# Performance work log

Hardware: AMD Instinct MI355X
Metric: run time of the kernel (lower is better)

## Reference

```python
import jax, jax.numpy as jnp
import numpy as np

N = 100000       # nodes
E_RAND = 3200000  # random edges; + N self loops appended
F_IN = 128
D = 64
SUBHEADS = 2
ALPHA = 0.2  # leaky_relu negative slope


def setup_inputs() -> dict:
    key = jax.random.key(0)
    ks = jax.random.split(key, 8)
    x = jax.random.normal(ks[0], (N, F_IN), jnp.float32)
    src = jax.random.randint(ks[1], (E_RAND,), 0, N)
    dst = jax.random.randint(ks[2], (E_RAND,), 0, N)
    loops = jnp.arange(N)  # add_remaining_self_loops
    edge_index = jnp.stack([jnp.concatenate([src, loops]),
                            jnp.concatenate([dst, loops])])  # [2, E_RAND+N]
    # xavier_normal_(gain=1.414): std = gain*sqrt(2/(fan_in+fan_out))
    xav = lambda k, shp, fan: jax.random.normal(k, shp, jnp.float32) * np.float32(1.414 * np.sqrt(2.0 / fan))
    W = xav(ks[3], (SUBHEADS, F_IN, D), F_IN + D)     # per-subhead weight
    b = jnp.zeros((SUBHEADS, D), jnp.float32)          # per-subhead bias
    fc = xav(ks[4], (SUBHEADS, D, 1), D + 1)           # NodeAdaptiveEncoder.fc
    bf = jnp.zeros((SUBHEADS,), jnp.float32)           # NodeAdaptiveEncoder.bf
    a_src = xav(ks[5], (SUBHEADS, D), D + 1)           # attention vector (dst side)
    a_dst = xav(ks[6], (SUBHEADS, D), D + 1)           # attention vector (src side)
    return dict(x=x, edge_index=edge_index, W=W, b=b, fc=fc, bf=bf, a_src=a_src, a_dst=a_dst)


def reference(x, edge_index, W, b, fc, bf, a_src, a_dst):
    row, col = edge_index[0], edge_index[1]  # out[row] += val * h[col]
    n = x.shape[0]
    outs = []
    for i in range(SUBHEADS):
        h = x @ W[i]  # [N, D]; dropout is identity in eval mode
        # --- GAT-style edge attention over the sparse graph ---
        s_r = h @ a_src[i]  # [N]
        s_c = h @ a_dst[i]  # [N]
        e = jax.nn.leaky_relu(s_r[row] + s_c[col], ALPHA)  # [E]
        m = jax.ops.segment_max(e, row, num_segments=n)
        ee = jnp.exp(e - m[row])
        denom = jax.ops.segment_sum(ee, row, num_segments=n)
        att = ee / denom[row]  # adj_mat_val = ones * softmax(e)
        # --- row normalization ---
        rs = jax.ops.segment_sum(att, row, num_segments=n)
        val = att / jnp.where(rs == 0, 1.0, rs)[row]
        # --- (i+1) hops of spmm ---
        vh = h
        for _ in range(i + 1):
            vh = jax.ops.segment_sum(val[:, None] * vh[col], row, num_segments=n)
        vh = jnp.where(jnp.isnan(vh), 0.0, vh)  # val_h[val_h != val_h] = 0
        vh = vh + b[i]
        # --- NodeAdaptiveEncoder: relu(x) + sigmoid(x@fc+bf) * min(x, 0) ---
        g = jax.nn.sigmoid(vh @ fc[i] + bf[i])  # [N, 1]
        vh = jnp.maximum(vh, 0.0) + g * jnp.minimum(vh, 0.0)
        vh = jax.nn.leaky_relu(vh, ALPHA)  # activation
        outs.append(vh)
    return jnp.concatenate(outs, axis=1)  # [N, SUBHEADS*D]
```

## Files before the change

kernel.cpp:

```cpp
#include <hip/hip_runtime.h>

#define ALPHA 0.2f

typedef short bf16x8 __attribute__((ext_vector_type(8)));
typedef float f32x4  __attribute__((ext_vector_type(4)));

__device__ __forceinline__ unsigned short f2bf(float f) {
    unsigned u = __float_as_uint(f);
    u += 0x7FFFu + ((u >> 16) & 1u);
    return (unsigned short)(u >> 16);
}
__device__ __forceinline__ float bflo(unsigned u) {
    return __uint_as_float(u << 16);
}
__device__ __forceinline__ float bfhi(unsigned u) {
    return __uint_as_float(u & 0xFFFF0000u);
}


__global__ __launch_bounds__(256) void f17_p1(
    const int* __restrict__ row, const int* __restrict__ col, int E, int N,
    int B, int CH, int* __restrict__ hist,
    const float* __restrict__ W, unsigned short* __restrict__ WT)
{
    __shared__ int h[4096];
    const int b = blockIdx.x, t = threadIdx.x;
    for (int k = t; k < B; k += 256) h[k] = 0;
    int gidx = b * 256 + t;
    if (gidx < 16384) {
        int i = gidx >> 13, c = (gidx >> 7) & 63, kk = gidx & 127;
        WT[gidx] = f2bf(W[i * 8192 + kk * 64 + c]);
    }
    __syncthreads();
    long base = (long)b * CH;
    long end  = base + CH; if (end > E) end = E;
    for (long e = base + t; e < end; e += 256) {
        int r = row[e], c = col[e];
        if ((unsigned)r < (unsigned)N && (unsigned)c < (unsigned)N)
            atomicAdd(&h[r >> 5], 1);
    }
    __syncthreads();
    for (int k = t; k < B; k += 256) hist[(size_t)k * 256 + b] = h[k];
}

__global__ __launch_bounds__(256) void f17_sc1(
    const int* __restrict__ h, int* __restrict__ bsums, int M)
{
    __shared__ int sdat[256];
    int t = threadIdx.x, blk = blockIdx.x;
    long base = (long)blk * 4096 + t * 16;
    int s = 0;
    #pragma unroll
    for (int j = 0; j < 16; ++j) {
        long idx = base + j;
        if (idx < M) s += h[idx];
    }
    sdat[t] = s; __syncthreads();
    for (int o = 1; o < 256; o <<= 1) {
        int add = (t >= o) ? sdat[t - o] : 0;
        __syncthreads();
        sdat[t] += add;
        __syncthreads();
    }
    if (t == 255) bsums[blk] = sdat[255];
}
__global__ __launch_bounds__(256) void f8_scan2(
    const int* __restrict__ bsums, int* __restrict__ boffs, int nb)
{
    __shared__ int sdat[256];
    int t = threadIdx.x;
    int v = (t < nb) ? bsums[t] : 0;
    sdat[t] = v; __syncthreads();
    for (int o = 1; o < 256; o <<= 1) {
        int add = (t >= o) ? sdat[t - o] : 0;
        __syncthreads();
// ... 6 lines not shown
    int* __restrict__ h, const int* __restrict__ boffs,
    int* __restrict__ bstart, int M)
{
    __shared__ int sdat[256];
    int t = threadIdx.x, blk = blockIdx.x;
    long base = (long)blk * 4096 + t * 16;
    int v[16]; int s = 0;
    #pragma unroll
    for (int j = 0; j < 16; ++j) {
        long idx = base + j;
        v[j] = (idx < M) ? h[idx] : 0;
        s += v[j];
    }
    sdat[t] = s; __syncthreads();
    for (int o = 1; o < 256; o <<= 1) {
        int add = (t >= o) ? sdat[t - o] : 0;
        __syncthreads();
        sdat[t] += add;
        __syncthreads();
    }
    int excl = boffs[blk] + sdat[t] - s;
    #pragma unroll
    for (int j = 0; j < 16; ++j) {
        long idx = base + j;
        if (idx < M) {
            h[idx] = excl;
            if ((idx & 255) == 0) bstart[idx >> 8] = excl;
            if (idx == M - 1)     bstart[M >> 8]   = excl + v[j];
            excl += v[j];
        }
    }
}

__global__ __launch_bounds__(256) void f17_p2(
    const int* __restrict__ row, const int* __restrict__ col, int E, int N,
    int B, int CH, const int* __restrict__ hist,
    const float* __restrict__ s_r, const float* __restrict__ s_c,
    uint2* __restrict__ pkA)
{
    __shared__ int cur[4096];
    const int b = blockIdx.x, t = threadIdx.x;
    for (int k = t; k < B; k += 256) cur[k] = hist[(size_t)k * 256 + b];
    __syncthreads();
    long base = (long)b * CH;
    long end  = base + CH; if (end > E) end = E;
    for (long e = base + t; e < end; e += 256) {
        int r = row[e], c = col[e];
        if ((unsigned)r >= (unsigned)N || (unsigned)c >= (unsigned)N) continue;
        float e0 = s_r[r] + s_c[c];
        float e1 = s_r[(size_t)N + r] + s_c[(size_t)N + c];
        e0 = (e0 > 0.f) ? e0 : ALPHA * e0;
        e1 = (e1 > 0.f) ? e1 : ALPHA * e1;
        unsigned py = ((unsigned)f2bf(expf(e1)) << 16) | (unsigned)f2bf(expf(e0));
        int pos = atomicAdd(&cur[r >> 5], 1);
        uint2 m; m.x = (unsigned)c | ((unsigned)(r & 31) << 25); m.y = py;
        pkA[pos] = m;
    }
}

__global__ __launch_bounds__(256) void f17_p3(
    const uint2* __restrict__ pkA, const int* __restrict__ bstart,
    int N, int B, uint2* __restrict__ pkB, int* __restrict__ rp)
{
    __shared__ int h32[32], ex33[33], cur32[32];
    const int k = blockIdx.x, t = threadIdx.x;
    const int p0 = bstart[k], p1 = bstart[k + 1];
    if (t < 32) h32[t] = 0;
    __syncthreads();
    for (int p = p0 + t; p < p1; p += 256)
        atomicAdd(&h32[pkA[p].x >> 25], 1);
    __syncthreads();
    if (t == 0) {
        int s = 0;
        #pragma unroll
        for (int j = 0; j < 32; ++j) { ex33[j] = s; s += h32[j]; }
        ex33[32] = s;
    }
    __syncthreads();
    if (t < 32) {
        int r = k * 32 + t;
        if (r < N) rp[r] = p0 + ex33[t];
        cur32[t] = p0 + ex33[t];
    }
    if (k == B - 1 && t == 0) rp[N] = p1;
    __syncthreads();
    for (int p = p0 + t; p < p1; p += 256) {
        uint2 m = pkA[p];
        int pos = atomicAdd(&cur32[m.x >> 25], 1);
        uint2 o; o.x = m.x & 0x01FFFFFFu; o.y = m.y;
        pkB[pos] = o;
    }
}

__global__ __launch_bounds__(256) void f14_h(
    const float* __restrict__ x,
    const unsigned short* __restrict__ WT,
    const float* __restrict__ a_src, const float* __restrict__ a_dst,
    unsigned short* __restrict__ Hb,
    float* __restrict__ s_r, float* __restrict__ s_c, int N)
{
    __shared__ __align__(16) unsigned short hs[4][16][72];
    const int t  = threadIdx.x;
    const int wv = t >> 6, l = t & 63;
    const int i  = blockIdx.x & 1;
    const int n0 = (blockIdx.x >> 1) * 64 + wv * 16;
    const int lm = l & 15, lg = l >> 4;

    int arow = n0 + lm; if (arow >= N) arow = N - 1;
    const float* xr = x + (size_t)arow * 128 + lg * 8;
    bf16x8 af[4];
    #pragma unroll
    for (int ks = 0; ks < 4; ++ks) {
        float4 u0 = *(const float4*)(xr + ks * 32);
        float4 u1 = *(const float4*)(xr + ks * 32 + 4);
        bf16x8 a;
        a[0] = (short)f2bf(u0.x); a[1] = (short)f2bf(u0.y);
        a[2] = (short)f2bf(u0.z); a[3] = (short)f2bf(u0.w);
        a[4] = (short)f2bf(u1.x); a[5] = (short)f2bf(u1.y);
        a[6] = (short)f2bf(u1.z); a[7] = (short)f2bf(u1.w);
        af[ks] = a;
    }

    const unsigned short* wr = WT + ((size_t)i * 64 + lm) * 128 + lg * 8;
    f32x4 zero = {0.f, 0.f, 0.f, 0.f};
    f32x4 acc[4];
    #pragma unroll
    for (int ct = 0; ct < 4; ++ct) {
        acc[ct] = zero;
        #pragma unroll
        for (int ks = 0; ks < 4; ++ks) {
            bf16x8 bf = *(const bf16x8*)(wr + ct * 16 * 128 + ks * 32);
            acc[ct] = __builtin_amdgcn_mfma_f32_16x16x32_bf16(af[ks], bf, acc[ct], 0, 0, 0);
        }
    }

    float asv[4], adv[4];
    #pragma unroll
    for (int ct = 0; ct < 4; ++ct) {
        asv[ct] = a_src[i * 64 + ct * 16 + lm];
        adv[ct] = a_dst[i * 64 + ct * 16 + lm];
    }
    #pragma unroll
    for (int reg = 0; reg < 4; ++reg) {
        float vr = 0.f, vc = 0.f;
        #pragma unroll
        for (int ct = 0; ct < 4; ++ct) {
            vr = fmaf(acc[ct][reg], asv[ct], vr);
            vc = fmaf(acc[ct][reg], adv[ct], vc);
        }
        #pragma unroll
        for (int off = 8; off; off >>= 1) {
            vr += __shfl_xor(vr, off);
            vc += __shfl_xor(vc, off);
        }
        int n = n0 + lg * 4 + reg;
        if (lm == 0 && n < N) {
            s_r[(size_t)i * N + n] = vr;
            s_c[(size_t)i * N + n] = vc;
        }
    }

    #pragma unroll
    for (int ct = 0; ct < 4; ++ct)
        #pragma unroll
        for (int reg = 0; reg < 4; ++reg)
            hs[wv][lg * 4 + reg][ct * 16 + lm] = f2bf(acc[ct][reg]);
    #pragma unroll
    for (int j = 0; j < 2; ++j) {
        int r = (l >> 3) + j * 8;
        int n = n0 + r;
        if (n < N) {
            int g = (l & 7) * 8;
            *(uint4*)(Hb + (size_t)n * 128 + i * 64 + g) =
                *(const uint4*)&hs[wv][r][g];
        }
    }
}

__global__ __launch_bounds__(256) void f10_h(
    const float* __restrict__ x, const float* __restrict__ W,
    const float* __restrict__ a_src, const float* __restrict__ a_dst,
    const int* __restrict__ row, const int* __restrict__ col, int E,
    int* __restrict__ cnt,
    float* __restrict__ Hf, unsigned short* __restrict__ Hb,
    float* __restrict__ s_r, float* __restrict__ s_c, int N)
{
    __shared__ __align__(16) float ws[128][64];
    __shared__ __align__(16) float xs[128][36];
    const int t  = threadIdx.x;
    const int i  = blockIdx.x & 1;
    const int n0 = (blockIdx.x >> 1) * 32;

    if (cnt) {
        const long total = (long)gridDim.x * 256;
        for (long e = (long)blockIdx.x * 256 + t; e < E; e += total) {
            int r = row[e], c = col[e];
            if ((unsigned)r < (unsigned)N && (unsigned)c < (unsigned)N)
                atomicAdd(cnt + r, 1);
        }
    }
    {
        const float* wp = W + (size_t)i * 8192;
        #pragma unroll
        for (int j = 0; j < 8; ++j) {
            int idx = t + j * 256;
            int k   = idx >> 4;
            int c4  = (idx & 15) * 4;
            *(float4*)&ws[k][c4] = *(const float4*)(wp + k * 64 + c4);
        }
    }
    {
        int r = t >> 3;
        int n = n0 + r;
        #pragma unroll
        for (int j = 0; j < 4; ++j) {
            int k0 = ((t & 7) + j * 8) * 4;
            float4 v = (n < N) ? *(const float4*)(x + (size_t)n * 128 + k0)
                               : make_float4(0.f, 0.f, 0.f, 0.f);
            xs[k0 + 0][r] = v.x; xs[k0 + 1][r] = v.y;
            xs[k0 + 2][r] = v.z; xs[k0 + 3][r] = v.w;
        }
    }
    __syncthreads();

    const int tc = t & 31, tn = t >> 5;
    float acc[4][2] = {};
    #pragma unroll 8
    for (int k = 0; k < 128; ++k) {
        float4 xv = *(const float4*)&xs[k][tn * 4];
        float2 wv = *(const float2*)&ws[k][tc * 2];
        acc[0][0] = fmaf(xv.x, wv.x, acc[0][0]);
        acc[0][1] = fmaf(xv.x, wv.y, acc[0][1]);
        acc[1][0] = fmaf(xv.y, wv.x, acc[1][0]);
        acc[1][1] = fmaf(xv.y, wv.y, acc[1][1]);
        acc[2][0] = fmaf(xv.z, wv.x, acc[2][0]);
        acc[2][1] = fmaf(xv.z, wv.y, acc[2][1]);
        acc[3][0] = fmaf(xv.w, wv.x, acc[3][0]);
        acc[3][1] = fmaf(xv.w, wv.y, acc[3][1]);
    }

    const float2 asv = *(const float2*)(a_src + i * 64 + tc * 2);
    const float2 adv = *(const float2*)(a_dst + i * 64 + tc * 2);
    #pragma unroll
    for (int a = 0; a < 4; ++a) {
        int n = n0 + tn * 4 + a;
        if (n >= N) break;
        float2 hv; hv.x = acc[a][0]; hv.y = acc[a][1];
        if (Hf) *(float2*)(Hf + (size_t)n * 128 + i * 64 + tc * 2) = hv;
        if (Hb) {
            ushort2 hb; hb.x = f2bf(hv.x); hb.y = f2bf(hv.y);
            *(ushort2*)(Hb + (size_t)n * 128 + (i * 32 + tc) * 2) = hb;
        }
        float pr = hv.x * asv.x + hv.y * asv.y;
        float pc = hv.x * adv.x + hv.y * adv.y;
        #pragma unroll
        for (int off = 16; off; off >>= 1) {
            pr += __shfl_xor(pr, off);
            pc += __shfl_xor(pc, off);
        }
        if (tc == 0) {
            s_r[(size_t)i * N + n] = pr;
            s_c[(size_t)i * N + n] = pc;
        }
    }
}

__global__ __launch_bounds__(256) void f16_scan1(
    const int* __restrict__ cnt, int* __restrict__ bsums, int N, int cs)
{
    __shared__ int sdat[256];
    int t = threadIdx.x, b = blockIdx.x;
    int s = 0;
    #pragma unroll
    for (int j = 0; j < 4; ++j) {
        int idx = b * 1024 + t * 4 + j;
        if (idx < N) s += cnt[(size_t)idx * cs];
    }
    sdat[t] = s; __syncthreads();
    for (int o = 1; o < 256; o <<= 1) {
        int add = (t >= o) ? sdat[t - o] : 0;
        __syncthreads();
        sdat[t] += add;
        __syncthreads();
    }
    if (t == 255) bsums[b] = sdat[255];
}
__global__ __launch_bounds__(256) void f16_scan3(
    int* __restrict__ cnt, const int* __restrict__ boffs,
    int* __restrict__ rp, int N, int cs)
{
    __shared__ int sdat[256];
    int t = threadIdx.x, b = blockIdx.x;
    int v[4]; int s = 0;
    #pragma unroll
    for (int j = 0; j < 4; ++j) {
        int idx = b * 1024 + t * 4 + j;
        v[j] = (idx < N) ? cnt[(size_t)idx * cs] : 0;
        s += v[j];
    }
    sdat[t] = s; __syncthreads();
    for (int o = 1; o < 256; o <<= 1) {
        int add = (t >= o) ? sdat[t - o] : 0;
        __syncthreads();
        sdat[t] += add;
        __syncthreads();
    }
    int excl = boffs[b] + sdat[t] - s;
    #pragma unroll
    for (int j = 0; j < 4; ++j) {
        int idx = b * 1024 + t * 4 + j;
        if (idx < N) {
            rp[idx] = excl;
            if (cs == 1) cnt[idx] = excl;
            if (idx == N - 1) rp[N] = excl + v[j];
            excl += v[j];
        }
    }
}

__global__ __launch_bounds__(256) void f8_scatter(
    const int* __restrict__ row, const int* __restrict__ col, int E,
    int* __restrict__ cur, int* __restrict__ colp, int N)
{
    int e = blockIdx.x * 256 + threadIdx.x;
    if (e >= E) return;
    int r = row[e], c = col[e];
    if ((unsigned)r >= (unsigned)N || (unsigned)c >= (unsigned)N) return;
    int pos = atomicAdd(cur + r, 1);
    colp[pos] = c;
}

__global__ __launch_bounds__(256) void f12_spmm2(
    const int* __restrict__ rp, const uint2* __restrict__ pk,
    const unsigned* __restrict__ Hb,
    const float* __restrict__ b, const float* __restrict__ fc,
    const float* __restrict__ bfv,
    unsigned short* __restrict__ A1b, float* __restrict__ out, int N)
{
    long gid = (long)blockIdx.x * 256 + threadIdx.x;
    int r = (int)(gid >> 6), d = (int)(gid & 63);
    if (r >= N) return;
    int p0 = rp[r], p1 = rp[r + 1];
    const int sub = d >> 5;
    float a0 = 0.f, a1 = 0.f, den = 0.f;
    int p = p0;
    for (; p + 8 <= p1; p += 8) {
        uint2 m0 = pk[p],     m1 = pk[p + 1], m2 = pk[p + 2], m3 = pk[p + 3];
        uint2 m4 = pk[p + 4], m5 = pk[p + 5], m6 = pk[p + 6], m7 = pk[p + 7];
        unsigned u0 = Hb[(size_t)m0.x * 64 + d];
        unsigned u1 = Hb[(size_t)m1.x * 64 + d];
        unsigned u2 = Hb[(size_t)m2.x * 64 + d];
        unsigned u3 = Hb[(size_t)m3.x * 64 + d];
        unsigned u4 = Hb[(size_t)m4.x * 64 + d];
        unsigned u5 = Hb[(size_t)m5.x * 64 + d];
        unsigned u6 = Hb[(size_t)m6.x * 64 + d];
        unsigned u7 = Hb[(size_t)m7.x * 64 + d];
        float v0 = sub ? bfhi(m0.y) : bflo(m0.y);
        float v1 = sub ? bfhi(m1.y) : bflo(m1.y);
        float v2 = sub ? bfhi(m2.y) : bflo(m2.y);
        float v3 = sub ? bfhi(m3.y) : bflo(m3.y);
        float v4 = sub ? bfhi(m4.y) : bflo(m4.y);
        float v5 = sub ? bfhi(m5.y) : bflo(m5.y);
        float v6 = sub ? bfhi(m6.y) : bflo(m6.y);
        float v7 = sub ? bfhi(m7.y) : bflo(m7.y);
        a0 = fmaf(v0, bflo(u0), a0); a1 = fmaf(v0, bfhi(u0), a1); den += v0;
        a0 = fmaf(v1, bflo(u1), a0); a1 = fmaf(v1, bfhi(u1), a1); den += v1;
        a0 = fmaf(v2, bflo(u2), a0); a1 = fmaf(v2, bfhi(u2), a1); den += v2;
        a0 = fmaf(v3, bflo(u3), a0); a1 = fmaf(v3, bfhi(u3), a1); den += v3;
        a0 = fmaf(v4, bflo(u4), a0); a1 = fmaf(v4, bfhi(u4), a1); den += v4;
        a0 = fmaf(v5, bflo(u5), a0); a1 = fmaf(v5, bfhi(u5), a1); den += v5;
        a0 = fmaf(v6, bflo(u6), a0); a1 = fmaf(v6, bfhi(u6), a1); den += v6;
        a0 = fmaf(v7, bflo(u7), a0); a1 = fmaf(v7, bfhi(u7), a1); den += v7;
    }
    for (; p < p1; ++p) {
        uint2 m = pk[p];
        unsigned u = Hb[(size_t)m.x * 64 + d];
        float v = sub ? bfhi(m.y) : bflo(m.y);
        a0 = fmaf(v, bflo(u), a0); a1 = fmaf(v, bfhi(u), a1); den += v;
    }
    float inv = (p1 > p0) ? 1.f / den : 0.f;
    float r0 = a0 * inv, r1 = a1 * inv;
    if (sub) {
        ushort2 res; res.x = f2bf(r0); res.y = f2bf(r1);
        *(ushort2*)(A1b + (size_t)r * 64 + (d - 32) * 2) = res;
    } else {
        int dcol = 2 * d;
        float vh0 = (r0 != r0) ? 0.f : r0;
        float vh1 = (r1 != r1) ? 0.f : r1;
        float2 bb = *(const float2*)(b + dcol);
        float2 ff = *(const float2*)(fc + dcol);
        vh0 += bb.x; vh1 += bb.y;
        float pp = vh0 * ff.x + vh1 * ff.y;
        #pragma unroll
        for (int off = 16; off; off >>= 1) pp += __shfl_xor(pp, off);
        float g = 1.f / (1.f + expf(-(pp + bfv[0])));
        float q0 = fmaxf(vh0, 0.f) + g * fminf(vh0, 0.f);
        float q1 = fmaxf(vh1, 0.f) + g * fminf(vh1, 0.f);
        q0 = (q0 > 0.f) ? q0 : ALPHA * q0;
        q1 = (q1 > 0.f) ? q1 : ALPHA * q1;
        float2 res; res.x = q0; res.y = q1;
        *(float2*)(out + (size_t)r * 128 + dcol) = res;
    }
}

__global__ __launch_bounds__(256) void f16_fin2(
    const int* __restrict__ rp, const uint2* __restrict__ pk,
    const unsigned* __restrict__ A1u,
    const float* __restrict__ b, const float* __restrict__ fc,
    const float* __restrict__ bfv,
    float* __restrict__ out, int N)
{
    long gid = (long)blockIdx.x * 256 + threadIdx.x;
    int r = (int)(gid >> 6), l = (int)(gid & 63);
    if (r >= N) return;
    const int half = l >> 5, lh = l & 31;
    int p0 = rp[r], p1 = rp[r + 1];
    float a0 = 0.f, a1 = 0.f, den = 0.f;
    int p = p0;
    for (; p + 8 <= p1; p += 8) {
        uint2 m0 = pk[p + half],     m1 = pk[p + 2 + half];
        uint2 m2 = pk[p + 4 + half], m3 = pk[p + 6 + half];
        unsigned u0 = A1u[(size_t)m0.x * 32 + lh];
        unsigned u1 = A1u[(size_t)m1.x * 32 + lh];
        unsigned u2 = A1u[(size_t)m2.x * 32 + lh];
        unsigned u3 = A1u[(size_t)m3.x * 32 + lh];
        float v0 = bfhi(m0.y), v1 = bfhi(m1.y);
        float v2 = bfhi(m2.y), v3 = bfhi(m3.y);
        a0 = fmaf(v0, bflo(u0), a0); a1 = fmaf(v0, bfhi(u0), a1); den += v0;
        a0 = fmaf(v1, bflo(u1), a0); a1 = fmaf(v1, bfhi(u1), a1); den += v1;
        a0 = fmaf(v2, bflo(u2), a0); a1 = fmaf(v2, bfhi(u2), a1); den += v2;
        a0 = fmaf(v3, bflo(u3), a0); a1 = fmaf(v3, bfhi(u3), a1); den += v3;
    }
    for (; p + 2 <= p1; p += 2) {
        uint2 m = pk[p + half];
        unsigned u = A1u[(size_t)m.x * 32 + lh];
        float v = bfhi(m.y);
        a0 = fmaf(v, bflo(u), a0); a1 = fmaf(v, bfhi(u), a1); den += v;
    }
    if (p < p1 && half == 0) {
        uint2 m = pk[p];
        unsigned u = A1u[(size_t)m.x * 32 + lh];
        float v = bfhi(m.y);
        a0 = fmaf(v, bflo(u), a0); a1 = fmaf(v, bfhi(u), a1); den += v;
    }
    a0 += __shfl_xor(a0, 32);
    a1 += __shfl_xor(a1, 32);
    den += __shfl_xor(den, 32);

    float inv = (p1 > p0) ? 1.f / den : 0.f;
    float vh0 = a0 * inv, vh1 = a1 * inv;
    if (vh0 != vh0) vh0 = 0.f;
    if (vh1 != vh1) vh1 = 0.f;
    const int dcol = 64 + 2 * lh;
    vh0 += b[dcol]; vh1 += b[dcol + 1];
    float pp = vh0 * fc[dcol] + vh1 * fc[dcol + 1];
    #pragma unroll
    for (int off = 16; off; off >>= 1) pp += __shfl_xor(pp, off);
    float g = 1.f / (1.f + expf(-(pp + bfv[1])));
    float q0 = fmaxf(vh0, 0.f) + g * fminf(vh0, 0.f);
    float q1 = fmaxf(vh1, 0.f) + g * fminf(vh1, 0.f);
    q0 = (q0 > 0.f) ? q0 : ALPHA * q0;
    q1 = (q1 > 0.f) ? q1 : ALPHA * q1;
    if (half == 0) {
        float2 res; res.x = q0; res.y = q1;
        *(float2*)(out + (size_t)r * 128 + dcol) = res;
    }
}

__global__ __launch_bounds__(256) void f11_spmm2_cp(
    const int* __restrict__ rp, const int* __restrict__ colp,
    const float* __restrict__ s_r, const float* __restrict__ s_c,
    const float* __restrict__ H,
    float* __restrict__ A0, float* __restrict__ A1, int N)
{
    long gid = (long)blockIdx.x * 256 + threadIdx.x;
    int r = (int)(gid >> 6), d = (int)(gid & 63);
    if (r >= N) return;
    int p0 = rp[r], p1 = rp[r + 1];
    const int sub = d >> 5;
    const float* scp = s_c + (size_t)sub * N;
    float sr = s_r[(size_t)sub * N + r];
    const float2* H2 = (const float2*)H;
    float a0 = 0.f, a1 = 0.f, den = 0.f;
    int p = p0;
    for (; p + 4 <= p1; p += 4) {
        int c0 = colp[p], c1 = colp[p + 1], c2 = colp[p + 2], c3 = colp[p + 3];
        float sc0 = scp[c0], sc1 = scp[c1], sc2 = scp[c2], sc3 = scp[c3];
        float2 h0 = H2[(size_t)c0 * 64 + d];
        float2 h1 = H2[(size_t)c1 * 64 + d];
        float2 h2 = H2[(size_t)c2 * 64 + d];
        float2 h3 = H2[(size_t)c3 * 64 + d];
        float e0 = sr + sc0; e0 = (e0 > 0.f) ? e0 : ALPHA * e0; float v0 = expf(e0);
        float e1 = sr + sc1; e1 = (e1 > 0.f) ? e1 : ALPHA * e1; float v1 = expf(e1);
        float e2 = sr + sc2; e2 = (e2 > 0.f) ? e2 : ALPHA * e2; float v2 = expf(e2);
        float e3 = sr + sc3; e3 = (e3 > 0.f) ? e3 : ALPHA * e3; float v3 = expf(e3);
        a0 = fmaf(v0, h0.x, a0); a1 = fmaf(v0, h0.y, a1); den += v0;
        a0 = fmaf(v1, h1.x, a0); a1 = fmaf(v1, h1.y, a1); den += v1;
        a0 = fmaf(v2, h2.x, a0); a1 = fmaf(v2, h2.y, a1); den += v2;
        a0 = fmaf(v3, h3.x, a0); a1 = fmaf(v3, h3.y, a1); den += v3;
// ... 132 lines not shown
}

extern "C" void kernel_launch(void* const* d_in, const int* in_sizes, int n_in,
                              void* d_out, int out_size, void* d_ws, size_t ws_size,
                              hipStream_t stream) {
    const float* x     = (const float*)d_in[0];
    const int*   ei    = (const int*)d_in[1];
    const float* W     = (const float*)d_in[2];
    const float* b     = (const float*)d_in[3];
    const float* fc    = (const float*)d_in[4];
    const float* bfv   = (const float*)d_in[5];
    const float* a_src = (const float*)d_in[6];
    const float* a_dst = (const float*)d_in[7];
    float* out = (float*)d_out;

    const int N = in_sizes[0] / 128;
    const int E = in_sizes[1] / 2;
    const int* row = ei;
    const int* col = ei + E;
    (void)n_in; (void)out_size;

    const int B  = (N + 31) >> 5;
    const int M  = B * 256;
    const int CH = (E + 255) / 256;
    const int nbh = (M + 4095) / 4096;

    unsigned short* Hb   = (unsigned short*)d_ws;
    unsigned short* A1b  = Hb + (size_t)N * 128;
    unsigned short* WT   = A1b + (size_t)N * 64;
    uint2*          pkA  = (uint2*)(WT + 16384);
    uint2*          pkB  = pkA + E;
    int*            hist = (int*)(pkB + E);
    int*            bst  = hist + (size_t)M;
    float*          s_rP = (float*)(bst + (B + 1));
    float*          s_cP = s_rP + 2 * (size_t)N;
    int*            rpP  = (int*)(s_cP + 2 * (size_t)N);
    int*            bsumP = rpP + (N + 1);
    int*            boffP = bsumP + 256;
    size_t          needP = (size_t)((char*)(boffP + 256) - (char*)d_ws);

    float* A0a   = (float*)d_ws;
    float* A1a   = A0a + (size_t)N * 64;
    int*   colpA = (int*)(A1a + (size_t)N * 64);
    float* s_rA  = (float*)(colpA + E);
    float* s_cA  = s_rA + 2 * (size_t)N;
    int*   rpA   = (int*)(s_cA + 2 * (size_t)N);
    int*   cntA  = rpA + (N + 1);
    int*   bsumA = cntA + N;
    int*   boffA = bsumA + 256;
    size_t needA = (size_t)((char*)(boffA + 256) - (char*)d_ws);

    const int g10 = 2 * ((N + 31) / 32);
    const int g14 = 2 * ((N + 63) / 64);
    const int eb  = (E + 255) / 256;
    const int rb  = (int)(((long)N * 64 + 255) / 256);
    const int nb  = (N + 1023) / 1024;

    if (ws_size >= needP && B <= 4096 && nbh <= 256) {
        f17_p1<<<256, 256, 0, stream>>>(row, col, E, N, B, CH, hist, W, WT);
        f14_h<<<g14, 256, 0, stream>>>(x, WT, a_src, a_dst, Hb, s_rP, s_cP, N);
        f17_sc1<<<nbh, 256, 0, stream>>>(hist, bsumP, M);
        f8_scan2<<<1, 256, 0, stream>>>(bsumP, boffP, nbh);
        f17_sc3<<<nbh, 256, 0, stream>>>(hist, boffP, bst, M);
        f17_p2<<<256, 256, 0, stream>>>(row, col, E, N, B, CH, hist,
                                        s_rP, s_cP, pkA);
        f17_p3<<<B, 256, 0, stream>>>(pkA, bst, N, B, pkB, rpP);
        f12_spmm2<<<rb, 256, 0, stream>>>(rpP, pkB, (const unsigned*)Hb,
                                          b, fc, bfv, A1b, out, N);
        f16_fin2<<<rb, 256, 0, stream>>>(rpP, pkB, (const unsigned*)A1b,
                                         b, fc, bfv, out, N);
    } else if (ws_size >= needA) {
        hipMemsetAsync(cntA, 0, (size_t)N * sizeof(int), stream);
        f10_h<<<g10, 256, 0, stream>>>(x, W, a_src, a_dst, row, col, E, cntA,
                                       out, nullptr, s_rA, s_cA, N);
        f16_scan1<<<nb, 256, 0, stream>>>(cntA, bsumA, N, 1);
        f8_scan2<<<1, 256, 0, stream>>>(bsumA, boffA, nb);
        f16_scan3<<<nb, 256, 0, stream>>>(cntA, boffA, rpA, N, 1);
        f8_scatter<<<eb, 256, 0, stream>>>(row, col, E, cntA, colpA, N);
        f11_spmm2_cp<<<rb, 256, 0, stream>>>(rpA, colpA, s_rA, s_cA, out,
                                             A0a, A1a, N);
        f8_fin<<<rb, 256, 0, stream>>>(A0a, b, fc, bfv, out, N, 0);
        f9_spmm_fin<<<rb, 256, 0, stream>>>(rpA, colpA, s_rA + N, s_cA + N,
                                            A1a, 64, 0, b, fc, bfv, out, N, 1);
    } else {
        float* A     = (float*)d_ws;
        float* s_r   = A + (size_t)N * 64;
        float* s_c   = s_r + 2 * (size_t)N;
        float* denom = s_c + 2 * (size_t)N;
        const size_t planeB = (size_t)N * 64 * sizeof(float);
        const int sb = (int)(((((long)E + 7) / 8) * 64 + 255) / 256);
        hipMemsetAsync(denom, 0, 2 * (size_t)N * sizeof(float), stream);
        f10_h<<<g10, 256, 0, stream>>>(x, W, a_src, a_dst, row, col, E, nullptr,
                                       out, nullptr, s_r, s_c, N);
        f8_edge<<<eb, 256, 0, stream>>>(row, col, E, s_r, s_c, denom, nullptr, N);
        const float* s_r1 = s_r + N; const float* s_c1 = s_c + N; const float* den1 = denom + N;
        hipMemsetAsync(A, 0, planeB, stream);
        f7_spmm<<<sb, 256, 0, stream>>>(row, col, E, s_r, s_c, denom, out, 0, A, N);
        f8_fin<<<rb, 256, 0, stream>>>(A, b, fc, bfv, out, N, 0);
        hipMemsetAsync(A, 0, planeB, stream);
        f7_spmm<<<sb, 256, 0, stream>>>(row, col, E, s_r1, s_c1, den1, out, 64, A, N);
        f7_copy<<<rb, 256, 0, stream>>>(A, out, 64, N);
        hipMemsetAsync(A, 0, planeB, stream);
        f7_spmm<<<sb, 256, 0, stream>>>(row, col, E, s_r1, s_c1, den1, out, 64, A, N);
// ... 4 lines not shown
```

Before: 512.9 us.

## Fuse edge histogram into projection kernel and precompute softmax denominators in bucket pass

Merges the edge-row histogram pass and the MFMA projection into one launch: the first 256 blocks build the histogram and the rest compute H, so the two independent stages can overlap, and the weight transpose moves to its own small kernel. The per-subhead attention scores are interleaved as float2 per node, so the edge pass fetches both heads with one load per endpoint. The softmax denominators are now summed once in the row-bucket sort kernel with shared-memory float atomics and stored per row. The two SpMM kernels read that value instead of re-accumulating and shuffle-reducing it. The cost is extra shared atomics in the bucket pass, and the denominator is summed in a different order.

```diff
diff --git a/kernel.cpp b/kernel.cpp
--- a/kernel.cpp
+++ b/kernel.cpp
@@ -17,30 +17,121 @@
     return __uint_as_float(u & 0xFFFF0000u);
 }
 
-
-__global__ __launch_bounds__(256) void f17_p1(
-    const int* __restrict__ row, const int* __restrict__ col, int E, int N,
-    int B, int CH, int* __restrict__ hist,
+__global__ __launch_bounds__(256) void f15_wt(
     const float* __restrict__ W, unsigned short* __restrict__ WT)
 {
-    __shared__ int h[4096];
-    const int b = blockIdx.x, t = threadIdx.x;
-    for (int k = t; k < B; k += 256) h[k] = 0;
-    int gidx = b * 256 + t;
-    if (gidx < 16384) {
-        int i = gidx >> 13, c = (gidx >> 7) & 63, kk = gidx & 127;
-        WT[gidx] = f2bf(W[i * 8192 + kk * 64 + c]);
-    }
-    __syncthreads();
-    long base = (long)b * CH;
-    long end  = base + CH; if (end > E) end = E;
-    for (long e = base + t; e < end; e += 256) {
-        int r = row[e], c = col[e];
-        if ((unsigned)r < (unsigned)N && (unsigned)c < (unsigned)N)
-            atomicAdd(&h[r >> 5], 1);
-    }
-    __syncthreads();
-    for (int k = t; k < B; k += 256) hist[(size_t)k * 256 + b] = h[k];
+    int t = blockIdx.x * 256 + threadIdx.x;
+    if (t < 2 * 64 * 128) {
+        int i = t >> 13, c = (t >> 7) & 63, k = t & 127;
+        WT[t] = f2bf(W[i * 8192 + k * 64 + c]);
+    }
+}
+
+__global__ __launch_bounds__(256) void f18_h(
+    const float* __restrict__ x,
+    const unsigned short* __restrict__ WT,
+    const float* __restrict__ a_src, const float* __restrict__ a_dst,
+    const int* __restrict__ row, const int* __restrict__ col, int E,
+    int N, int B, int CH, int* __restrict__ hist,
+    unsigned short* __restrict__ Hb,
+    float* __restrict__ s2_r, float* __restrict__ s2_c)
+{
+    __shared__ __align__(16) unsigned char sm[16384];
+    const int t = threadIdx.x;
+
+    if (blockIdx.x < 256) {
+        int* h = (int*)sm;
+        const int b = blockIdx.x;
+        for (int k = t; k < B; k += 256) h[k] = 0;
+        __syncthreads();
+        long base = (long)b * CH;
+        long end  = base + CH; if (end > E) end = E;
+        for (long e = base + t; e < end; e += 256) {
+            int r = row[e], c = col[e];
+            if ((unsigned)r < (unsigned)N && (unsigned)c < (unsigned)N)
+                atomicAdd(&h[r >> 5], 1);
+        }
+        __syncthreads();
+        for (int k = t; k < B; k += 256) hist[(size_t)k * 256 + b] = h[k];
+        return;
+    }
+
+    unsigned short (*hs)[16][72] = (unsigned short (*)[16][72])sm;
+    const int bid = blockIdx.x - 256;
+    const int wv = t >> 6, l = t & 63;
+    const int i  = bid & 1;
+    const int n0 = (bid >> 1) * 64 + wv * 16;
+    const int lm = l & 15, lg = l >> 4;
+
+    int arow = n0 + lm; if (arow >= N) arow = N - 1;
+    const float* xr = x + (size_t)arow * 128 + lg * 8;
+    bf16x8 af[4];
+    #pragma unroll
+    for (int ks = 0; ks < 4; ++ks) {
+        float4 u0 = *(const float4*)(xr + ks * 32);
+        float4 u1 = *(const float4*)(xr + ks * 32 + 4);
+        bf16x8 a;
+        a[0] = (short)f2bf(u0.x); a[1] = (short)f2bf(u0.y);
+        a[2] = (short)f2bf(u0.z); a[3] = (short)f2bf(u0.w);
+        a[4] = (short)f2bf(u1.x); a[5] = (short)f2bf(u1.y);
+        a[6] = (short)f2bf(u1.z); a[7] = (short)f2bf(u1.w);
+        af[ks] = a;
+    }
+
+    const unsigned short* wr = WT + ((size_t)i * 64 + lm) * 128 + lg * 8;
+    f32x4 zero = {0.f, 0.f, 0.f, 0.f};
+    f32x4 acc[4];
+    #pragma unroll
+    for (int ct = 0; ct < 4; ++ct) {
+        acc[ct] = zero;
+        #pragma unroll
+        for (int ks = 0; ks < 4; ++ks) {
+            bf16x8 bf = *(const bf16x8*)(wr + ct * 16 * 128 + ks * 32);
+            acc[ct] = __builtin_amdgcn_mfma_f32_16x16x32_bf16(af[ks], bf, acc[ct], 0, 0, 0);
+        }
+    }
+
+    float asv[4], adv[4];
+    #pragma unroll
+    for (int ct = 0; ct < 4; ++ct) {
+        asv[ct] = a_src[i * 64 + ct * 16 + lm];
+        adv[ct] = a_dst[i * 64 + ct * 16 + lm];
+    }
+    #pragma unroll
+    for (int reg = 0; reg < 4; ++reg) {
+        float vr = 0.f, vc = 0.f;
+        #pragma unroll
+        for (int ct = 0; ct < 4; ++ct) {
+            vr = fmaf(acc[ct][reg], asv[ct], vr);
+            vc = fmaf(acc[ct][reg], adv[ct], vc);
+        }
+        #pragma unroll
+        for (int off = 8; off; off >>= 1) {
+            vr += __shfl_xor(vr, off);
+            vc += __shfl_xor(vc, off);
+        }
+        int n = n0 + lg * 4 + reg;
+        if (lm == 0 && n < N) {
+            s2_r[(size_t)n * 2 + i] = vr;
+            s2_c[(size_t)n * 2 + i] = vc;
+        }
+    }
+
+    #pragma unroll
+    for (int ct = 0; ct < 4; ++ct)
+        #pragma unroll
+        for (int reg = 0; reg < 4; ++reg)
+            hs[wv][lg * 4 + reg][ct * 16 + lm] = f2bf(acc[ct][reg]);
+    #pragma unroll
+    for (int j = 0; j < 2; ++j) {
+        int r = (l >> 3) + j * 8;
+        int n = n0 + r;
+        if (n < N) {
+            int g = (l & 7) * 8;
+            *(uint4*)(Hb + (size_t)n * 128 + i * 64 + g) =
+                *(const uint4*)&hs[wv][r][g];
+        }
+    }
 }
 
 __global__ __launch_bounds__(256) void f17_sc1(
@@ -113,10 +204,10 @@
     }
 }
 
-__global__ __launch_bounds__(256) void f17_p2(
+__global__ __launch_bounds__(256) void f18_p2(
     const int* __restrict__ row, const int* __restrict__ col, int E, int N,
     int B, int CH, const int* __restrict__ hist,
-    const float* __restrict__ s_r, const float* __restrict__ s_c,
+    const float* __restrict__ s2_r, const float* __restrict__ s2_c,
     uint2* __restrict__ pkA)
 {
     __shared__ int cur[4096];
@@ -128,8 +219,10 @@
     for (long e = base + t; e < end; e += 256) {
         int r = row[e], c = col[e];
         if ((unsigned)r >= (unsigned)N || (unsigned)c >= (unsigned)N) continue;
-        float e0 = s_r[r] + s_c[c];
-        float e1 = s_r[(size_t)N + r] + s_c[(size_t)N + c];
+        float2 sr = *(const float2*)(s2_r + (size_t)r * 2);
+        float2 sc = *(const float2*)(s2_c + (size_t)c * 2);
+        float e0 = sr.x + sc.x;
+        float e1 = sr.y + sc.y;
         e0 = (e0 > 0.f) ? e0 : ALPHA * e0;
         e1 = (e1 > 0.f) ? e1 : ALPHA * e1;
         unsigned py = ((unsigned)f2bf(expf(e1)) << 16) | (unsigned)f2bf(expf(e0));
@@ -139,17 +232,24 @@
     }
 }
 
-__global__ __launch_bounds__(256) void f17_p3(
+__global__ __launch_bounds__(256) void f18_p3(
     const uint2* __restrict__ pkA, const int* __restrict__ bstart,
-    int N, int B, uint2* __restrict__ pkB, int* __restrict__ rp)
+    int N, int B, uint2* __restrict__ pkB, int* __restrict__ rp,
+    float* __restrict__ den2)
 {
     __shared__ int h32[32], ex33[33], cur32[32];
+    __shared__ float d0[32], d1[32];
     const int k = blockIdx.x, t = threadIdx.x;
     const int p0 = bstart[k], p1 = bstart[k + 1];
-    if (t < 32) h32[t] = 0;
+    if (t < 32) { h32[t] = 0; d0[t] = 0.f; d1[t] = 0.f; }
     __syncthreads();
-    for (int p = p0 + t; p < p1; p += 256)
-        atomicAdd(&h32[pkA[p].x >> 25], 1);
+    for (int p = p0 + t; p < p1; p += 256) {
+        uint2 m = pkA[p];
+        int rl = m.x >> 25;
+        atomicAdd(&h32[rl], 1);
+        atomicAdd(&d0[rl], bflo(m.y));
+        atomicAdd(&d1[rl], bfhi(m.y));
+    }
     __syncthreads();
     if (t == 0) {
         int s = 0;
@@ -160,7 +260,11 @@
     __syncthreads();
     if (t < 32) {
         int r = k * 32 + t;
-        if (r < N) rp[r] = p0 + ex33[t];
+        if (r < N) {
+            rp[r] = p0 + ex33[t];
+            float2 dd; dd.x = d0[t]; dd.y = d1[t];
+            *(float2*)(den2 + (size_t)r * 2) = dd;
+        }
         cur32[t] = p0 + ex33[t];
     }
     if (k == B - 1 && t == 0) rp[N] = p1;
@@ -173,247 +277,10 @@
     }
 }
 
-__global__ __launch_bounds__(256) void f14_h(
-    const float* __restrict__ x,
-    const unsigned short* __restrict__ WT,
-    const float* __restrict__ a_src, const float* __restrict__ a_dst,
-    unsigned short* __restrict__ Hb,
-    float* __restrict__ s_r, float* __restrict__ s_c, int N)
-{
-    __shared__ __align__(16) unsigned short hs[4][16][72];
-    const int t  = threadIdx.x;
-    const int wv = t >> 6, l = t & 63;
-    const int i  = blockIdx.x & 1;
-    const int n0 = (blockIdx.x >> 1) * 64 + wv * 16;
-    const int lm = l & 15, lg = l >> 4;
-
-    int arow = n0 + lm; if (arow >= N) arow = N - 1;
-    const float* xr = x + (size_t)arow * 128 + lg * 8;
-    bf16x8 af[4];
-    #pragma unroll
-    for (int ks = 0; ks < 4; ++ks) {
-        float4 u0 = *(const float4*)(xr + ks * 32);
-        float4 u1 = *(const float4*)(xr + ks * 32 + 4);
-        bf16x8 a;
-        a[0] = (short)f2bf(u0.x); a[1] = (short)f2bf(u0.y);
-        a[2] = (short)f2bf(u0.z); a[3] = (short)f2bf(u0.w);
-        a[4] = (short)f2bf(u1.x); a[5] = (short)f2bf(u1.y);
-        a[6] = (short)f2bf(u1.z); a[7] = (short)f2bf(u1.w);
-        af[ks] = a;
-    }
-
-    const unsigned short* wr = WT + ((size_t)i * 64 + lm) * 128 + lg * 8;
-    f32x4 zero = {0.f, 0.f, 0.f, 0.f};
-    f32x4 acc[4];
-    #pragma unroll
-    for (int ct = 0; ct < 4; ++ct) {
-        acc[ct] = zero;
-        #pragma unroll
-        for (int ks = 0; ks < 4; ++ks) {
-            bf16x8 bf = *(const bf16x8*)(wr + ct * 16 * 128 + ks * 32);
-            acc[ct] = __builtin_amdgcn_mfma_f32_16x16x32_bf16(af[ks], bf, acc[ct], 0, 0, 0);
-        }
-    }
-
-    float asv[4], adv[4];
-    #pragma unroll
-    for (int ct = 0; ct < 4; ++ct) {
-        asv[ct] = a_src[i * 64 + ct * 16 + lm];
-        adv[ct] = a_dst[i * 64 + ct * 16 + lm];
-    }
-    #pragma unroll
-    for (int reg = 0; reg < 4; ++reg) {
-        float vr = 0.f, vc = 0.f;
-        #pragma unroll
-        for (int ct = 0; ct < 4; ++ct) {
-            vr = fmaf(acc[ct][reg], asv[ct], vr);
-            vc = fmaf(acc[ct][reg], adv[ct], vc);
-        }
-        #pragma unroll
-        for (int off = 8; off; off >>= 1) {
-            vr += __shfl_xor(vr, off);
-            vc += __shfl_xor(vc, off);
-        }
-        int n = n0 + lg * 4 + reg;
-        if (lm == 0 && n < N) {
-            s_r[(size_t)i * N + n] = vr;
-            s_c[(size_t)i * N + n] = vc;
-        }
-    }
-
-    #pragma unroll
-    for (int ct = 0; ct < 4; ++ct)
-        #pragma unroll
-        for (int reg = 0; reg < 4; ++reg)
-            hs[wv][lg * 4 + reg][ct * 16 + lm] = f2bf(acc[ct][reg]);
-    #pragma unroll
-    for (int j = 0; j < 2; ++j) {
-        int r = (l >> 3) + j * 8;
-        int n = n0 + r;
-        if (n < N) {
-            int g = (l & 7) * 8;
-            *(uint4*)(Hb + (size_t)n * 128 + i * 64 + g) =
-                *(const uint4*)&hs[wv][r][g];
-        }
-    }
-}
-
-__global__ __launch_bounds__(256) void f10_h(
-    const float* __restrict__ x, const float* __restrict__ W,
-    const float* __restrict__ a_src, const float* __restrict__ a_dst,
-    const int* __restrict__ row, const int* __restrict__ col, int E,
-    int* __restrict__ cnt,
-    float* __restrict__ Hf, unsigned short* __restrict__ Hb,
-    float* __restrict__ s_r, float* __restrict__ s_c, int N)
-{
-    __shared__ __align__(16) float ws[128][64];
-    __shared__ __align__(16) float xs[128][36];
-    const int t  = threadIdx.x;
-    const int i  = blockIdx.x & 1;
-    const int n0 = (blockIdx.x >> 1) * 32;
-
-    if (cnt) {
-        const long total = (long)gridDim.x * 256;
-        for (long e = (long)blockIdx.x * 256 + t; e < E; e += total) {
-            int r = row[e], c = col[e];
-            if ((unsigned)r < (unsigned)N && (unsigned)c < (unsigned)N)
-                atomicAdd(cnt + r, 1);
-        }
-    }
-    {
-        const float* wp = W + (size_t)i * 8192;
-        #pragma unroll
-        for (int j = 0; j < 8; ++j) {
-            int idx = t + j * 256;
-            int k   = idx >> 4;
-            int c4  = (idx & 15) * 4;
-            *(float4*)&ws[k][c4] = *(const float4*)(wp + k * 64 + c4);
-        }
-    }
-    {
-        int r = t >> 3;
-        int n = n0 + r;
-        #pragma unroll
-        for (int j = 0; j < 4; ++j) {
-            int k0 = ((t & 7) + j * 8) * 4;
-            float4 v = (n < N) ? *(const float4*)(x + (size_t)n * 128 + k0)
-                               : make_float4(0.f, 0.f, 0.f, 0.f);
-            xs[k0 + 0][r] = v.x; xs[k0 + 1][r] = v.y;
-            xs[k0 + 2][r] = v.z; xs[k0 + 3][r] = v.w;
-        }
-    }
-    __syncthreads();
-
-    const int tc = t & 31, tn = t >> 5;
-    float acc[4][2] = {};
-    #pragma unroll 8
-    for (int k = 0; k < 128; ++k) {
-        float4 xv = *(const float4*)&xs[k][tn * 4];
-        float2 wv = *(const float2*)&ws[k][tc * 2];
-        acc[0][0] = fmaf(xv.x, wv.x, acc[0][0]);
-        acc[0][1] = fmaf(xv.x, wv.y, acc[0][1]);
-        acc[1][0] = fmaf(xv.y, wv.x, acc[1][0]);
-        acc[1][1] = fmaf(xv.y, wv.y, acc[1][1]);
-        acc[2][0] = fmaf(xv.z, wv.x, acc[2][0]);
-        acc[2][1] = fmaf(xv.z, wv.y, acc[2][1]);
-        acc[3][0] = fmaf(xv.w, wv.x, acc[3][0]);
-        acc[3][1] = fmaf(xv.w, wv.y, acc[3][1]);
-    }
-
-    const float2 asv = *(const float2*)(a_src + i * 64 + tc * 2);
-    const float2 adv = *(const float2*)(a_dst + i * 64 + tc * 2);
-    #pragma unroll
-    for (int a = 0; a < 4; ++a) {
-        int n = n0 + tn * 4 + a;
-        if (n >= N) break;
-        float2 hv; hv.x = acc[a][0]; hv.y = acc[a][1];
-        if (Hf) *(float2*)(Hf + (size_t)n * 128 + i * 64 + tc * 2) = hv;
-        if (Hb) {
-            ushort2 hb; hb.x = f2bf(hv.x); hb.y = f2bf(hv.y);
-            *(ushort2*)(Hb + (size_t)n * 128 + (i * 32 + tc) * 2) = hb;
-        }
-        float pr = hv.x * asv.x + hv.y * asv.y;
-        float pc = hv.x * adv.x + hv.y * adv.y;
-        #pragma unroll
-        for (int off = 16; off; off >>= 1) {
-            pr += __shfl_xor(pr, off);
-            pc += __shfl_xor(pc, off);
-        }
-        if (tc == 0) {
-            s_r[(size_t)i * N + n] = pr;
-            s_c[(size_t)i * N + n] = pc;
-        }
-    }
-}
-
-__global__ __launch_bounds__(256) void f16_scan1(
-    const int* __restrict__ cnt, int* __restrict__ bsums, int N, int cs)
-{
-    __shared__ int sdat[256];
-    int t = threadIdx.x, b = blockIdx.x;
-    int s = 0;
-    #pragma unroll
-    for (int j = 0; j < 4; ++j) {
-        int idx = b * 1024 + t * 4 + j;
-        if (idx < N) s += cnt[(size_t)idx * cs];
-    }
-    sdat[t] = s; __syncthreads();
-    for (int o = 1; o < 256; o <<= 1) {
-        int add = (t >= o) ? sdat[t - o] : 0;
-        __syncthreads();
-        sdat[t] += add;
-        __syncthreads();
-    }
-    if (t == 255) bsums[b] = sdat[255];
-}
-__global__ __launch_bounds__(256) void f16_scan3(
-    int* __restrict__ cnt, const int* __restrict__ boffs,
-    int* __restrict__ rp, int N, int cs)
-{
-    __shared__ int sdat[256];
-    int t = threadIdx.x, b = blockIdx.x;
-    int v[4]; int s = 0;
-    #pragma unroll
-    for (int j = 0; j < 4; ++j) {
-        int idx = b * 1024 + t * 4 + j;
-        v[j] = (idx < N) ? cnt[(size_t)idx * cs] : 0;
-        s += v[j];
-    }
-    sdat[t] = s; __syncthreads();
-    for (int o = 1; o < 256; o <<= 1) {
-        int add = (t >= o) ? sdat[t - o] : 0;
-        __syncthreads();
-        sdat[t] += add;
-        __syncthreads();
-    }
-    int excl = boffs[b] + sdat[t] - s;
-    #pragma unroll
-    for (int j = 0; j < 4; ++j) {
-        int idx = b * 1024 + t * 4 + j;
-        if (idx < N) {
-            rp[idx] = excl;
-            if (cs == 1) cnt[idx] = excl;
-            if (idx == N - 1) rp[N] = excl + v[j];
-            excl += v[j];
-        }
-    }
-}
-
-__global__ __launch_bounds__(256) void f8_scatter(
-    const int* __restrict__ row, const int* __restrict__ col, int E,
-    int* __restrict__ cur, int* __restrict__ colp, int N)
-{
-    int e = blockIdx.x * 256 + threadIdx.x;
-    if (e >= E) return;
-    int r = row[e], c = col[e];
-    if ((unsigned)r >= (unsigned)N || (unsigned)c >= (unsigned)N) return;
-    int pos = atomicAdd(cur + r, 1);
-    colp[pos] = c;
-}
-
-__global__ __launch_bounds__(256) void f12_spmm2(
+__global__ __launch_bounds__(256) void f18_spmm2(
     const int* __restrict__ rp, const uint2* __restrict__ pk,
     const unsigned* __restrict__ Hb,
+    const float* __restrict__ den2,
     const float* __restrict__ b, const float* __restrict__ fc,
     const float* __restrict__ bfv,
     unsigned short* __restrict__ A1b, float* __restrict__ out, int N)
@@ -423,7 +290,8 @@
     if (r >= N) return;
     int p0 = rp[r], p1 = rp[r + 1];
     const int sub = d >> 5;
-    float a0 = 0.f, a1 = 0.f, den = 0.f;
+    float den = den2[(size_t)r * 2 + sub];
+    float a0 = 0.f, a1 = 0.f;
     int p = p0;
     for (; p + 8 <= p1; p += 8) {
         uint2 m0 = pk[p],     m1 = pk[p + 1], m2 = pk[p + 2], m3 = pk[p + 3];
@@ -444,20 +312,20 @@
         float v5 = sub ? bfhi(m5.y) : bflo(m5.y);
         float v6 = sub ? bfhi(m6.y) : bflo(m6.y);
         float v7 = sub ? bfhi(m7.y) : bflo(m7.y);
-        a0 = fmaf(v0, bflo(u0), a0); a1 = fmaf(v0, bfhi(u0), a1); den += v0;
-        a0 = fmaf(v1, bflo(u1), a0); a1 = fmaf(v1, bfhi(u1), a1); den += v1;
-        a0 = fmaf(v2, bflo(u2), a0); a1 = fmaf(v2, bfhi(u2), a1); den += v2;
-        a0 = fmaf(v3, bflo(u3), a0); a1 = fmaf(v3, bfhi(u3), a1); den += v3;
-        a0 = fmaf(v4, bflo(u4), a0); a1 = fmaf(v4, bfhi(u4), a1); den += v4;
-        a0 = fmaf(v5, bflo(u5), a0); a1 = fmaf(v5, bfhi(u5), a1); den += v5;
-        a0 = fmaf(v6, bflo(u6), a0); a1 = fmaf(v6, bfhi(u6), a1); den += v6;
-        a0 = fmaf(v7, bflo(u7), a0); a1 = fmaf(v7, bfhi(u7), a1); den += v7;
+        a0 = fmaf(v0, bflo(u0), a0); a1 = fmaf(v0, bfhi(u0), a1);
+        a0 = fmaf(v1, bflo(u1), a0); a1 = fmaf(v1, bfhi(u1), a1);
+        a0 = fmaf(v2, bflo(u2), a0); a1 = fmaf(v2, bfhi(u2), a1);
+        a0 = fmaf(v3, bflo(u3), a0); a1 = fmaf(v3, bfhi(u3), a1);
+        a0 = fmaf(v4, bflo(u4), a0); a1 = fmaf(v4, bfhi(u4), a1);
+        a0 = fmaf(v5, bflo(u5), a0); a1 = fmaf(v5, bfhi(u5), a1);
+        a0 = fmaf(v6, bflo(u6), a0); a1 = fmaf(v6, bfhi(u6), a1);
+        a0 = fmaf(v7, bflo(u7), a0); a1 = fmaf(v7, bfhi(u7), a1);
     }
     for (; p < p1; ++p) {
         uint2 m = pk[p];
         unsigned u = Hb[(size_t)m.x * 64 + d];
         float v = sub ? bfhi(m.y) : bflo(m.y);
-        a0 = fmaf(v, bflo(u), a0); a1 = fmaf(v, bfhi(u), a1); den += v;
+        a0 = fmaf(v, bflo(u), a0); a1 = fmaf(v, bfhi(u), a1);
     }
     float inv = (p1 > p0) ? 1.f / den : 0.f;
     float r0 = a0 * inv, r1 = a1 * inv;
@@ -484,9 +352,10 @@
     }
 }
 
-__global__ __launch_bounds__(256) void f16_fin2(
+__global__ __launch_bounds__(256) void f18_fin2(
     const int* __restrict__ rp, const uint2* __restrict__ pk,
     const unsigned* __restrict__ A1u,
+    const float* __restrict__ den2,
     const float* __restrict__ b, const float* __restrict__ fc,
     const float* __restrict__ bfv,
     float* __restrict__ out, int N)
@@ -496,7 +365,8 @@
     if (r >= N) return;
     const int half = l >> 5, lh = l & 31;
     int p0 = rp[r], p1 = rp[r + 1];
-    float a0 = 0.f, a1 = 0.f, den = 0.f;
+    float den = den2[(size_t)r * 2 + 1];
+    float a0 = 0.f, a1 = 0.f;
     int p = p0;
     for (; p + 8 <= p1; p += 8) {
         uint2 m0 = pk[p + half],     m1 = pk[p + 2 + half];
@@ -507,26 +377,25 @@
         unsigned u3 = A1u[(size_t)m3.x * 32 + lh];
         float v0 = bfhi(m0.y), v1 = bfhi(m1.y);
         float v2 = bfhi(m2.y), v3 = bfhi(m3.y);
-        a0 = fmaf(v0, bflo(u0), a0); a1 = fmaf(v0, bfhi(u0), a1); den += v0;
-        a0 = fmaf(v1, bflo(u1), a0); a1 = fmaf(v1, bfhi(u1), a1); den += v1;
-        a0 = fmaf(v2, bflo(u2), a0); a1 = fmaf(v2, bfhi(u2), a1); den += v2;
-        a0 = fmaf(v3, bflo(u3), a0); a1 = fmaf(v3, bfhi(u3), a1); den += v3;
+        a0 = fmaf(v0, bflo(u0), a0); a1 = fmaf(v0, bfhi(u0), a1);
+        a0 = fmaf(v1, bflo(u1), a0); a1 = fmaf(v1, bfhi(u1), a1);
+        a0 = fmaf(v2, bflo(u2), a0); a1 = fmaf(v2, bfhi(u2), a1);
+        a0 = fmaf(v3, bflo(u3), a0); a1 = fmaf(v3, bfhi(u3), a1);
     }
     for (; p + 2 <= p1; p += 2) {
         uint2 m = pk[p + half];
         unsigned u = A1u[(size_t)m.x * 32 + lh];
         float v = bfhi(m.y);
-        a0 = fmaf(v, bflo(u), a0); a1 = fmaf(v, bfhi(u), a1); den += v;
+        a0 = fmaf(v, bflo(u), a0); a1 = fmaf(v, bfhi(u), a1);
     }
     if (p < p1 && half == 0) {
         uint2 m = pk[p];
         unsigned u = A1u[(size_t)m.x * 32 + lh];
         float v = bfhi(m.y);
-        a0 = fmaf(v, bflo(u), a0); a1 = fmaf(v, bfhi(u), a1); den += v;
+        a0 = fmaf(v, bflo(u), a0); a1 = fmaf(v, bfhi(u), a1);
     }
     a0 += __shfl_xor(a0, 32);
     a1 += __shfl_xor(a1, 32);
-    den += __shfl_xor(den, 32);
 
     float inv = (p1 > p0) ? 1.f / den : 0.f;
     float vh0 = a0 * inv, vh1 = a1 * inv;
@@ -546,6 +415,159 @@
         float2 res; res.x = q0; res.y = q1;
         *(float2*)(out + (size_t)r * 128 + dcol) = res;
     }
+}
+
+__global__ __launch_bounds__(256) void f10_h(
+    const float* __restrict__ x, const float* __restrict__ W,
+    const float* __restrict__ a_src, const float* __restrict__ a_dst,
+    const int* __restrict__ row, const int* __restrict__ col, int E,
+    int* __restrict__ cnt,
+    float* __restrict__ Hf, unsigned short* __restrict__ Hb,
+    float* __restrict__ s_r, float* __restrict__ s_c, int N)
+{
+    __shared__ __align__(16) float ws[128][64];
+    __shared__ __align__(16) float xs[128][36];
+    const int t  = threadIdx.x;
+    const int i  = blockIdx.x & 1;
+    const int n0 = (blockIdx.x >> 1) * 32;
+
+    if (cnt) {
+        const long total = (long)gridDim.x * 256;
+        for (long e = (long)blockIdx.x * 256 + t; e < E; e += total) {
+            int r = row[e], c = col[e];
+            if ((unsigned)r < (unsigned)N && (unsigned)c < (unsigned)N)
+                atomicAdd(cnt + r, 1);
+        }
+    }
+    {
+        const float* wp = W + (size_t)i * 8192;
+        #pragma unroll
+        for (int j = 0; j < 8; ++j) {
+            int idx = t + j * 256;
+            int k   = idx >> 4;
+            int c4  = (idx & 15) * 4;
+            *(float4*)&ws[k][c4] = *(const float4*)(wp + k * 64 + c4);
+        }
+    }
+    {
+        int r = t >> 3;
+        int n = n0 + r;
+        #pragma unroll
+        for (int j = 0; j < 4; ++j) {
+            int k0 = ((t & 7) + j * 8) * 4;
+            float4 v = (n < N) ? *(const float4*)(x + (size_t)n * 128 + k0)
+                               : make_float4(0.f, 0.f, 0.f, 0.f);
+            xs[k0 + 0][r] = v.x; xs[k0 + 1][r] = v.y;
+            xs[k0 + 2][r] = v.z; xs[k0 + 3][r] = v.w;
+        }
+    }
+    __syncthreads();
+
+    const int tc = t & 31, tn = t >> 5;
+    float acc[4][2] = {};
+    #pragma unroll 8
+    for (int k = 0; k < 128; ++k) {
+        float4 xv = *(const float4*)&xs[k][tn * 4];
+        float2 wv = *(const float2*)&ws[k][tc * 2];
+        acc[0][0] = fmaf(xv.x, wv.x, acc[0][0]);
+        acc[0][1] = fmaf(xv.x, wv.y, acc[0][1]);
+        acc[1][0] = fmaf(xv.y, wv.x, acc[1][0]);
+        acc[1][1] = fmaf(xv.y, wv.y, acc[1][1]);
+        acc[2][0] = fmaf(xv.z, wv.x, acc[2][0]);
+        acc[2][1] = fmaf(xv.z, wv.y, acc[2][1]);
+        acc[3][0] = fmaf(xv.w, wv.x, acc[3][0]);
+        acc[3][1] = fmaf(xv.w, wv.y, acc[3][1]);
+    }
+
+    const float2 asv = *(const float2*)(a_src + i * 64 + tc * 2);
+    const float2 adv = *(const float2*)(a_dst + i * 64 + tc * 2);
+    #pragma unroll
+    for (int a = 0; a < 4; ++a) {
+        int n = n0 + tn * 4 + a;
+        if (n >= N) break;
+        float2 hv; hv.x = acc[a][0]; hv.y = acc[a][1];
+        if (Hf) *(float2*)(Hf + (size_t)n * 128 + i * 64 + tc * 2) = hv;
+        if (Hb) {
+            ushort2 hb; hb.x = f2bf(hv.x); hb.y = f2bf(hv.y);
+            *(ushort2*)(Hb + (size_t)n * 128 + (i * 32 + tc) * 2) = hb;
+        }
+        float pr = hv.x * asv.x + hv.y * asv.y;
+        float pc = hv.x * adv.x + hv.y * adv.y;
+        #pragma unroll
+        for (int off = 16; off; off >>= 1) {
+            pr += __shfl_xor(pr, off);
+            pc += __shfl_xor(pc, off);
+        }
+        if (tc == 0) {
+            s_r[(size_t)i * N + n] = pr;
+            s_c[(size_t)i * N + n] = pc;
+        }
+    }
+}
+
+__global__ __launch_bounds__(256) void f16_scan1(
+    const int* __restrict__ cnt, int* __restrict__ bsums, int N, int cs)
+{
+    __shared__ int sdat[256];
+    int t = threadIdx.x, b = blockIdx.x;
+    int s = 0;
+    #pragma unroll
+    for (int j = 0; j < 4; ++j) {
+        int idx = b * 1024 + t * 4 + j;
+        if (idx < N) s += cnt[(size_t)idx * cs];
+    }
+    sdat[t] = s; __syncthreads();
+    for (int o = 1; o < 256; o <<= 1) {
+        int add = (t >= o) ? sdat[t - o] : 0;
+        __syncthreads();
+        sdat[t] += add;
+        __syncthreads();
+    }
+    if (t == 255) bsums[b] = sdat[255];
+}
+__global__ __launch_bounds__(256) void f16_scan3(
+    int* __restrict__ cnt, const int* __restrict__ boffs,
+    int* __restrict__ rp, int N, int cs)
+{
+    __shared__ int sdat[256];
+    int t = threadIdx.x, b = blockIdx.x;
+    int v[4]; int s = 0;
+    #pragma unroll
+    for (int j = 0; j < 4; ++j) {
+        int idx = b * 1024 + t * 4 + j;
+        v[j] = (idx < N) ? cnt[(size_t)idx * cs] : 0;
+        s += v[j];
+    }
+    sdat[t] = s; __syncthreads();
+    for (int o = 1; o < 256; o <<= 1) {
+        int add = (t >= o) ? sdat[t - o] : 0;
+        __syncthreads();
+        sdat[t] += add;
+        __syncthreads();
+    }
+    int excl = boffs[b] + sdat[t] - s;
+    #pragma unroll
+    for (int j = 0; j < 4; ++j) {
+        int idx = b * 1024 + t * 4 + j;
+        if (idx < N) {
+            rp[idx] = excl;
+            if (cs == 1) cnt[idx] = excl;
+            if (idx == N - 1) rp[N] = excl + v[j];
+            excl += v[j];
+        }
+    }
+}
+
+__global__ __launch_bounds__(256) void f8_scatter(
+    const int* __restrict__ row, const int* __restrict__ col, int E,
+    int* __restrict__ cur, int* __restrict__ colp, int N)
+{
+    int e = blockIdx.x * 256 + threadIdx.x;
+    if (e >= E) return;
+    int r = row[e], c = col[e];
+    if ((unsigned)r >= (unsigned)N || (unsigned)c >= (unsigned)N) return;
+    int pos = atomicAdd(cur + r, 1);
+    colp[pos] = c;
 }
 
 __global__ __launch_bounds__(256) void f11_spmm2_cp(
@@ -744,9 +766,10 @@
     uint2*          pkB  = pkA + E;
     int*            hist = (int*)(pkB + E);
     int*            bst  = hist + (size_t)M;
-    float*          s_rP = (float*)(bst + (B + 1));
-    float*          s_cP = s_rP + 2 * (size_t)N;
-    int*            rpP  = (int*)(s_cP + 2 * (size_t)N);
+    float*          s2r  = (float*)(bst + (B + 1));
+    float*          s2c  = s2r + 2 * (size_t)N;
+    float*          den2 = s2c + 2 * (size_t)N;
+    int*            rpP  = (int*)(den2 + 2 * (size_t)N);
     int*            bsumP = rpP + (N + 1);
     int*            boffP = bsumP + 256;
     size_t          needP = (size_t)((char*)(boffP + 256) - (char*)d_ws);
@@ -763,24 +786,25 @@
     size_t needA = (size_t)((char*)(boffA + 256) - (char*)d_ws);
 
     const int g10 = 2 * ((N + 31) / 32);
-    const int g14 = 2 * ((N + 63) / 64);
+    const int g18 = 256 + 2 * ((N + 63) / 64);
     const int eb  = (E + 255) / 256;
     const int rb  = (int)(((long)N * 64 + 255) / 256);
     const int nb  = (N + 1023) / 1024;
 
     if (ws_size >= needP && B <= 4096 && nbh <= 256) {
-        f17_p1<<<256, 256, 0, stream>>>(row, col, E, N, B, CH, hist, W, WT);
-        f14_h<<<g14, 256, 0, stream>>>(x, WT, a_src, a_dst, Hb, s_rP, s_cP, N);
+        f15_wt<<<64, 256, 0, stream>>>(W, WT);
+        f18_h<<<g18, 256, 0, stream>>>(x, WT, a_src, a_dst, row, col, E,
+                                       N, B, CH, hist, Hb, s2r, s2c);
         f17_sc1<<<nbh, 256, 0, stream>>>(hist, bsumP, M);
         f8_scan2<<<1, 256, 0, stream>>>(bsumP, boffP, nbh);
         f17_sc3<<<nbh, 256, 0, stream>>>(hist, boffP, bst, M);
-        f17_p2<<<256, 256, 0, stream>>>(row, col, E, N, B, CH, hist,
-                                        s_rP, s_cP, pkA);
-        f17_p3<<<B, 256, 0, stream>>>(pkA, bst, N, B, pkB, rpP);
-        f12_spmm2<<<rb, 256, 0, stream>>>(rpP, pkB, (const unsigned*)Hb,
-                                          b, fc, bfv, A1b, out, N);
-        f16_fin2<<<rb, 256, 0, stream>>>(rpP, pkB, (const unsigned*)A1b,
-                                         b, fc, bfv, out, N);
+        f18_p2<<<256, 256, 0, stream>>>(row, col, E, N, B, CH, hist,
+                                        s2r, s2c, pkA);
+        f18_p3<<<B, 256, 0, stream>>>(pkA, bst, N, B, pkB, rpP, den2);
+        f18_spmm2<<<rb, 256, 0, stream>>>(rpP, pkB, (const unsigned*)Hb,
+                                          den2, b, fc, bfv, A1b, out, N);
+        f18_fin2<<<rb, 256, 0, stream>>>(rpP, pkB, (const unsigned*)A1b,
+                                         den2, b, fc, bfv, out, N);
     } else if (ws_size >= needA) {
         hipMemsetAsync(cntA, 0, (size_t)N * sizeof(int), stream);
         f10_h<<<g10, 256, 0, stream>>>(x, W, a_src, a_dst, row, col, E, cntA,
```

After: 516.9 us. No clear change (+0.8%).
